# Performance work log

Hardware: AMD Instinct MI355X
Metric: run time of the kernel (lower is better)

## Reference

```python
import jax, jax.numpy as jnp
import numpy as np

AUDIO_DIM, TEXT_DIM, HIDDEN_DIM = 512, 768, 512
B, AUDIO_LEN, TEXT_LEN = 8, 2048, 512


def setup_inputs() -> dict:
    key = jax.random.key(0)
    ks = jax.random.split(key, 9)
    audio_features = jax.random.normal(ks[0], (B, AUDIO_LEN, AUDIO_DIM), dtype=jnp.float32)
    text_features = jax.random.normal(ks[1], (B, TEXT_LEN, TEXT_DIM), dtype=jnp.float32)
    text_mask = jax.random.randint(ks[2], (B, TEXT_LEN), 0, 2).astype(jnp.int32)
    # Linear params (PyTorch default init scale ~ U(-1/sqrt(fan_in), 1/sqrt(fan_in)))
    def lin(kw, kb, fan_in, fan_out):
        bound = 1.0 / np.sqrt(fan_in)
        W = jax.random.uniform(kw, (fan_in, fan_out), minval=-bound, maxval=bound, dtype=jnp.float32)
        b = jax.random.uniform(kb, (fan_out,), minval=-bound, maxval=bound, dtype=jnp.float32)
        return W, b
    Wq, bq = lin(ks[3], ks[4], AUDIO_DIM, HIDDEN_DIM)
    Wk, bk = lin(ks[5], ks[6], TEXT_DIM, HIDDEN_DIM)
    Wv, bv = lin(ks[7], ks[8], TEXT_DIM, HIDDEN_DIM)
    return {
        "audio_features": audio_features,
        "text_features": text_features,
        "Wq": Wq, "bq": bq, "Wk": Wk, "bk": bk, "Wv": Wv, "bv": bv,
        "text_mask": text_mask,
    }


def reference(audio_features, text_features, Wq, bq, Wk, bk, Wv, bv, text_mask):
    scale = HIDDEN_DIM ** -0.5
    q = jnp.einsum("bad,dh->bah", audio_features, Wq) + bq  # (B, A, H)
    k = jnp.einsum("btd,dh->bth", text_features, Wk) + bk   # (B, T, H)
    v = jnp.einsum("btd,dh->bth", text_features, Wv) + bv   # (B, T, H)
    scores = jnp.einsum("bah,bth->bat", q, k) * scale        # (B, A, T)
    mask = text_mask[:, None, :]  # (B, 1, T)
    scores = jnp.where(mask == 0, -jnp.inf, scores)
    attn = jax.nn.softmax(scores, axis=-1)
    # dropout is identity in eval mode
    enhanced_audio = jnp.einsum("bat,bth->bah", attn, v)     # (B, A, H)
    return enhanced_audio
```

## Files before the change

### kernel.cpp

```cpp
#include <hip/hip_runtime.h>
#include <cstdint>
#include <cstddef>

#define AUDIO_DIM 512
#define TEXT_DIM  768
#define HIDDEN    512
#define BATCH     8
#define ALEN      2048
#define TLEN      512

typedef _Float16 half8 __attribute__((ext_vector_type(8)));
typedef _Float16 half4_t __attribute__((ext_vector_type(4)));
typedef float floatx4 __attribute__((ext_vector_type(4)));

#define AS1 __attribute__((address_space(1)))
#define AS3 __attribute__((address_space(3)))

__device__ __forceinline__ void gload_lds16(const void* g, void* l) {
    __builtin_amdgcn_global_load_lds((const AS1 void*)g, (AS3 void*)l, 16, 0, 0);
}

__device__ __forceinline__ int swz(int r) { return (r >> 1) & 3; }

#define VMCNT(N) asm volatile("s_waitcnt vmcnt(" #N ")" ::: "memory")

__global__ __launch_bounds__(256) void prep(
    const float* __restrict__ text,
    const float* __restrict__ Wq, const float* __restrict__ Wk,
    const float* __restrict__ Wv,
    _Float16* __restrict__ text_h,
    _Float16* __restrict__ Wq_t, _Float16* __restrict__ Wk_t,
    _Float16* __restrict__ Wv_t)
{
    __shared__ _Float16 tt[32 * 33];
    const int bid = blockIdx.x, tid = threadIdx.x;
    if (bid < 3072) {
        int i = bid * 256 + tid;
        floatx4 v = __builtin_nontemporal_load(&((const floatx4*)text)[i]);
        half4_t h;
        h.x = (_Float16)v.x; h.y = (_Float16)v.y; h.z = (_Float16)v.z; h.w = (_Float16)v.w;
        ((half4_t*)text_h)[i] = h;
    } else {
        const float* src; _Float16* dst; int R, lb;
        if (bid < 3328)      { lb = bid - 3072; src = Wq; dst = Wq_t; R = 512; }
        else if (bid < 3712) { lb = bid - 3328; src = Wk; dst = Wk_t; R = 768; }
        else                 { lb = bid - 3712; src = Wv; dst = Wv_t; R = 768; }
        const int C = 512;
        const int c0 = (lb & 15) * 32, r0 = (lb >> 4) * 32;
        const int tx = tid & 31, ty = tid >> 5;
#pragma unroll
        for (int i = 0; i < 4; i++) {
            int r = ty + i * 8;
            tt[r * 33 + tx] =
                (_Float16)__builtin_nontemporal_load(&src[(size_t)(r0 + r) * C + c0 + tx]);
        }
        __syncthreads();
#pragma unroll
        for (int i = 0; i < 4; i++) {
            int r = ty + i * 8;
            dst[(size_t)(c0 + r) * R + r0 + tx] = tt[tx * 33 + r];
        }
    }
}

template <bool OUT16, bool ROWBIAS, bool CVT_A>
__device__ __forceinline__ void gemm_body(
    const void* __restrict__ Avp, const _Float16* __restrict__ Bt,
    const float* __restrict__ bias, void* __restrict__ Cp,
    int N, int K, int m0, int n0, _Float16* Asm, _Float16* Bsm)
{
    const int tid = threadIdx.x;
    const int l = tid & 63, w = tid >> 6;
    const int wm = w >> 1, wn = w & 1;
    const int srow = l >> 2, sj = l & 3;
    const int q = l >> 4, c16 = l & 15;

    floatx4 acc[4][4] = {};

    for (int k0 = 0; k0 < K; k0 += 32) {
        if (k0) __syncthreads();
#pragma unroll
        for (int i = 0; i < 2; i++) {
            int rb = (w * 2 + i) * 16;
            int r = rb + srow;
            int cc = sj ^ swz(r);
            if constexpr (CVT_A) {
                const float* Af = (const float*)Avp;
                const float* s = &Af[(size_t)(m0 + r) * K + k0 + cc * 8];
                floatx4 v0 = __builtin_nontemporal_load((const floatx4*)s);
                floatx4 v1 = __builtin_nontemporal_load((const floatx4*)(s + 4));
                half8 h;
                h[0] = (_Float16)v0.x; h[1] = (_Float16)v0.y;
                h[2] = (_Float16)v0.z; h[3] = (_Float16)v0.w;
                h[4] = (_Float16)v1.x; h[5] = (_Float16)v1.y;
                h[6] = (_Float16)v1.z; h[7] = (_Float16)v1.w;
                *(half8*)&Asm[r * 32 + sj * 8] = h;
            } else {
                const _Float16* Ah = (const _Float16*)Avp;
                gload_lds16(Ah + (size_t)(m0 + r) * K + k0 + cc * 8, Asm + rb * 32);
            }
            gload_lds16(Bt + (size_t)(n0 + r) * K + k0 + cc * 8, Bsm + rb * 32);
        }
        __syncthreads();

        half8 af[4], bf[4];
#pragma unroll
        for (int t = 0; t < 4; t++) {
            int rA = wm * 64 + t * 16 + c16;
            af[t] = *(const half8*)&Asm[rA * 32 + ((q ^ swz(rA)) << 3)];
            int rB = wn * 64 + t * 16 + c16;
            bf[t] = *(const half8*)&Bsm[rB * 32 + ((q ^ swz(rB)) << 3)];
        }
#pragma unroll
        for (int mi = 0; mi < 4; mi++)
#pragma unroll
            for (int ni = 0; ni < 4; ni++)
                acc[mi][ni] = __builtin_amdgcn_mfma_f32_16x16x32_f16(
                    af[mi], bf[ni], acc[mi][ni], 0, 0, 0);
    }

    if (OUT16) {
        float bcol[4];
        float brow[4][4];
        if (!ROWBIAS) {
#pragma unroll
            for (int ni = 0; ni < 4; ni++)
                bcol[ni] = bias[n0 + wn * 64 + ni * 16 + c16];
        } else {
#pragma unroll
            for (int mi = 0; mi < 4; mi++) {
                float4 b4 = *(const float4*)&bias[m0 + wm * 64 + mi * 16 + q * 4];
                brow[mi][0] = b4.x; brow[mi][1] = b4.y;
                brow[mi][2] = b4.z; brow[mi][3] = b4.w;
            }
        }
        _Float16* C = (_Float16*)Cp;
#pragma unroll
        for (int ni = 0; ni < 4; ni++) {
            int col = n0 + wn * 64 + ni * 16 + c16;
#pragma unroll
            for (int mi = 0; mi < 4; mi++) {
                int row = m0 + wm * 64 + mi * 16 + q * 4;
#pragma unroll
                for (int r = 0; r < 4; r++) {
                    float b = ROWBIAS ? brow[mi][r] : bcol[ni];
                    C[(size_t)(row + r) * N + col] = (_Float16)(acc[mi][ni][r] + b);
                }
            }
        }
    } else {
        float* C = (float*)Cp;
#pragma unroll
        for (int ni = 0; ni < 4; ni++) {
            int col = n0 + wn * 64 + ni * 16 + c16;
#pragma unroll
            for (int mi = 0; mi < 4; mi++) {
                int row = m0 + wm * 64 + mi * 16 + q * 4;
#pragma unroll
                for (int r = 0; r < 4; r++)
                    C[(size_t)(row + r) * N + col] = acc[mi][ni][r];
            }
        }
    }
}

__global__ __launch_bounds__(256, 3) void qkv_gemm(
    const float* __restrict__ audio, const _Float16* __restrict__ text_h,
    const _Float16* __restrict__ Wq_t, const _Float16* __restrict__ Wk_t,
    const _Float16* __restrict__ Wv_t,
    const float* __restrict__ bq, const float* __restrict__ bk,
    const float* __restrict__ bv,
    _Float16* __restrict__ Qh, _Float16* __restrict__ Kh,
    _Float16* __restrict__ Vt)
{
    __shared__ __align__(16) _Float16 Asm[128 * 32];
    __shared__ __align__(16) _Float16 Bsm[128 * 32];
    const int bid = blockIdx.x;
    if (bid < 512) {
        int t = (bid & 7) * 64 + (bid >> 3);
        gemm_body<true, false, true>(audio, Wq_t, bq, Qh, 512, 512,
                                     (t >> 2) * 128, (t & 3) * 128, Asm, Bsm);
    } else if (bid < 640) {
        int s = bid - 512;
        int t = (s & 7) * 16 + (s >> 3);
        gemm_body<true, false, false>(text_h, Wk_t, bk, Kh, 512, 768,
                                      (t >> 2) * 128, (t & 3) * 128, Asm, Bsm);
    } else {
        int s = bid - 640;
        int t = (s & 7) * 16 + (s >> 3);
        int z = t >> 4, by = (t >> 2) & 3, bx = t & 3;
        gemm_body<true, true, false>(Wv_t, text_h + (size_t)z * 393216, bv,
                                     Vt + (size_t)z * 262144, 512, 768,
                                     by * 128, bx * 128, Asm, Bsm);
    }
}

#define STAGE64(SRC, K0, BUF)                                               \
    do {                                                                    \
        _Pragma("unroll")                                                   \
        for (int i_ = 0; i_ < 4; i_++) {                                    \
            int lr_ = i_ * 16 + srow;                                       \
            int cc_ = sj ^ swz(lr_);                                        \
            gload_lds16((SRC) + (size_t)(w * 64 + lr_) * HIDDEN + (K0) + cc_ * 8, \
                        &(BUF)[i_ * 512]);                                  \
        }                                                                   \
    } while (0)

__global__ __launch_bounds__(512, 2) void attn(
    const _Float16* __restrict__ Qh, const _Float16* __restrict__ Kh,
    const _Float16* __restrict__ Vt, const int* __restrict__ mask,
    float* __restrict__ out)
{
    __shared__ __align__(16) _Float16 QPs[64 * 512];
    __shared__ __align__(16) _Float16 Ks[8][2][64 * 32];
    __shared__ float red[8][64];
    __shared__ float red2[8][64];
    const int tid = threadIdx.x, l = tid & 63, w = tid >> 6;
    const int lin = blockIdx.x;
    const int tb = (lin & 7) * 32 + (lin >> 3);
    const int b = tb >> 5, a0 = (tb & 31) * 64;
    const _Float16* Qb = Qh + (size_t)(b * ALEN + a0) * HIDDEN;
    const _Float16* Kb = Kh + (size_t)b * TLEN * HIDDEN;
    const _Float16* Vb = Vt + (size_t)b * TLEN * HIDDEN;
    const int srow = l >> 2, sj = l & 3;
    const int q = l >> 4, c16 = l & 15;

    int mv[4];
#pragma unroll
    for (int ni = 0; ni < 4; ni++)
        mv[ni] = mask[b * TLEN + w * 64 + ni * 16 + c16];

#pragma unroll
    for (int i = 0; i < 8; i++) {
        int r = w * 8 + i;
        gload_lds16(Qb + (size_t)r * 512 + ((l ^ (r & 7)) << 3), &QPs[r * 512]);
    }
    STAGE64(Kb, 0, Ks[w][0]);
    STAGE64(Kb, 32, Ks[w][1]);
    __syncthreads();

    floatx4 acc[4][4] = {};
#pragma unroll
    for (int ks = 0; ks < 16; ks++) {
        const int k0 = ks * 32;
        if (ks == 15) { VMCNT(0); } else { VMCNT(4); }
        half8 af[4], bf[4];
        const _Float16* kb = &Ks[w][ks & 1][0];
#pragma unroll
        for (int t = 0; t < 4; t++) {
            int rA = t * 16 + c16;
            af[t] = *(const half8*)&QPs[rA * 512 + ((((k0 >> 3) + q) ^ (rA & 7)) << 3)];
            bf[t] = *(const half8*)&kb[rA * 32 + ((q ^ swz(rA)) << 3)];
        }
#pragma unroll
        for (int mi = 0; mi < 4; mi++)
#pragma unroll
            for (int ni = 0; ni < 4; ni++)
                acc[mi][ni] = __builtin_amdgcn_mfma_f32_16x16x32_f16(
                    af[mi], bf[ni], acc[mi][ni], 0, 0, 0);
        if (ks < 14) STAGE64(Kb, k0 + 64, Ks[w][ks & 1]);
    }

    STAGE64(Vb, 0, Ks[w][0]);
    STAGE64(Vb, 32, Ks[w][1]);

    const float scale = 0.044194173824159216f;
#pragma unroll
    for (int mi = 0; mi < 4; mi++)
#pragma unroll
        for (int ni = 0; ni < 4; ni++)
#pragma unroll
            for (int r = 0; r < 4; r++)
                acc[mi][ni][r] = mv[ni] ? acc[mi][ni][r] * scale : -1e30f;

    float mx[4][4];
#pragma unroll
    for (int mi = 0; mi < 4; mi++)
#pragma unroll
        for (int r = 0; r < 4; r++) {
            float m = -1e30f;
#pragma unroll
            for (int ni = 0; ni < 4; ni++) m = fmaxf(m, acc[mi][ni][r]);
#pragma unroll
            for (int off = 1; off <= 8; off <<= 1) m = fmaxf(m, __shfl_xor(m, off));
            mx[mi][r] = m;
        }
    if (c16 == 0)
#pragma unroll
        for (int mi = 0; mi < 4; mi++)
#pragma unroll
            for (int r = 0; r < 4; r++) red[w][mi * 16 + q * 4 + r] = mx[mi][r];
    __syncthreads();
#pragma unroll
    for (int mi = 0; mi < 4; mi++)
#pragma unroll
        for (int r = 0; r < 4; r++) {
            int row = mi * 16 + q * 4 + r;
            float m = red[0][row];
#pragma unroll
            for (int ww = 1; ww < 8; ww++) m = fmaxf(m, red[ww][row]);
            mx[mi][r] = m;
        }

    float sm[4][4];
#pragma unroll
    for (int mi = 0; mi < 4; mi++)
#pragma unroll
        for (int r = 0; r < 4; r++) {
            float s = 0.f;
#pragma unroll
            for (int ni = 0; ni < 4; ni++) {
                float e = __expf(acc[mi][ni][r] - mx[mi][r]);
                acc[mi][ni][r] = e;
                s += e;
            }
#pragma unroll
            for (int off = 1; off <= 8; off <<= 1) s += __shfl_xor(s, off);
            sm[mi][r] = s;
        }
    if (c16 == 0)
#pragma unroll
        for (int mi = 0; mi < 4; mi++)
#pragma unroll
            for (int r = 0; r < 4; r++) red2[w][mi * 16 + q * 4 + r] = sm[mi][r];
    __syncthreads();

    _Float16* Ps = QPs;
#pragma unroll
    for (int mi = 0; mi < 4; mi++)
#pragma unroll
        for (int r = 0; r < 4; r++) {
            int row = mi * 16 + q * 4 + r;
            float s = red2[0][row];
#pragma unroll
            for (int ww = 1; ww < 8; ww++) s += red2[ww][row];
            float inv = 1.f / s;
#pragma unroll
            for (int ni = 0; ni < 4; ni++) {
                int col = w * 64 + ni * 16 + c16;
                Ps[row * 512 + ((((col >> 3) ^ (row & 7)) << 3) + (col & 7))] =
                    (_Float16)(acc[mi][ni][r] * inv);
            }
        }
    __syncthreads();

    floatx4 oacc[4][4] = {};
#pragma unroll
    for (int ts = 0; ts < 16; ts++) {
        const int t0 = ts * 32;
        if (ts == 15) { VMCNT(0); } else { VMCNT(4); }
        half8 af[4], bf[4];
        const _Float16* vb = &Ks[w][ts & 1][0];
#pragma unroll
        for (int t = 0; t < 4; t++) {
            int rA = t * 16 + c16;
            af[t] = *(const half8*)&Ps[rA * 512 + ((((t0 >> 3) + q) ^ (rA & 7)) << 3)];
            bf[t] = *(const half8*)&vb[rA * 32 + ((q ^ swz(rA)) << 3)];
        }
#pragma unroll
        for (int mi = 0; mi < 4; mi++)
#pragma unroll
            for (int ni = 0; ni < 4; ni++)
                oacc[mi][ni] = __builtin_amdgcn_mfma_f32_16x16x32_f16(
                    af[mi], bf[ni], oacc[mi][ni], 0, 0, 0);
        if (ts < 14) STAGE64(Vb, t0 + 64, Ks[w][ts & 1]);
    }

    float* Ob = out + (size_t)(b * ALEN + a0) * HIDDEN;
#pragma unroll
    for (int ni = 0; ni < 4; ni++) {
        int col = w * 64 + ni * 16 + c16;
#pragma unroll
        for (int mi = 0; mi < 4; mi++) {
            int row = mi * 16 + q * 4;
#pragma unroll
            for (int r = 0; r < 4; r++)
                __builtin_nontemporal_store(oacc[mi][ni][r],
                                            &Ob[(size_t)(row + r) * HIDDEN + col]);
        }
    }
}

extern "C" void kernel_launch(void* const* d_in, const int* in_sizes, int n_in,
                              void* d_out, int out_size, void* d_ws, size_t ws_size,
                              hipStream_t stream)
{
    const float* audio = (const float*)d_in[0];
    const float* text  = (const float*)d_in[1];
    const float* Wq    = (const float*)d_in[2];
    const float* bq    = (const float*)d_in[3];
    const float* Wk    = (const float*)d_in[4];
    const float* bk    = (const float*)d_in[5];
    const float* Wv    = (const float*)d_in[6];
    const float* bv    = (const float*)d_in[7];
    const int*   maskp = (const int*)d_in[8];
    float* out = (float*)d_out;

    _Float16* Qh = (_Float16*)d_out + (size_t)8388608;

    _Float16* ws16   = (_Float16*)d_ws;
    _Float16* text_h = ws16;
    _Float16* Wq_t   = text_h + 3145728;
    _Float16* Wk_t   = Wq_t + 262144;
    _Float16* Wv_t   = Wk_t + 393216;
    _Float16* Kh     = Wv_t + 393216;
    _Float16* Vt     = Kh + 2097152;

    prep<<<4096, 256, 0, stream>>>(text, Wq, Wk, Wv,
                                   text_h, Wq_t, Wk_t, Wv_t);
    qkv_gemm<<<768, 256, 0, stream>>>(audio, text_h, Wq_t, Wk_t, Wv_t,
                                      bq, bk, bv, Qh, Kh, Vt);
    attn<<<256, 512, 0, stream>>>(Qh, Kh, Vt, maskp, out);
}
```

Baseline: 167.5 us.

## Use 128x256 tiles for Q projection and pack K/V tiles two per block

```diff
diff --git a/kernel.cpp b/kernel.cpp
--- a/kernel.cpp
+++ b/kernel.cpp
@@ -63,13 +63,12 @@
     }
 }
 
-template <bool OUT16, bool ROWBIAS, bool CVT_A>
+template <bool OUT16, bool ROWBIAS>
 __device__ __forceinline__ void gemm_body(
-    const void* __restrict__ Avp, const _Float16* __restrict__ Bt,
+    const _Float16* __restrict__ A, const _Float16* __restrict__ Bt,
     const float* __restrict__ bias, void* __restrict__ Cp,
-    int N, int K, int m0, int n0, _Float16* Asm, _Float16* Bsm)
-{
-    const int tid = threadIdx.x;
+    int N, int K, int m0, int n0, _Float16* Asm, _Float16* Bsm, int tid)
+{
     const int l = tid & 63, w = tid >> 6;
     const int wm = w >> 1, wn = w & 1;
     const int srow = l >> 2, sj = l & 3;
@@ -84,21 +83,7 @@
             int rb = (w * 2 + i) * 16;
             int r = rb + srow;
             int cc = sj ^ swz(r);
-            if constexpr (CVT_A) {
-                const float* Af = (const float*)Avp;
-                const float* s = &Af[(size_t)(m0 + r) * K + k0 + cc * 8];
-                floatx4 v0 = __builtin_nontemporal_load((const floatx4*)s);
-                floatx4 v1 = __builtin_nontemporal_load((const floatx4*)(s + 4));
-                half8 h;
-                h[0] = (_Float16)v0.x; h[1] = (_Float16)v0.y;
-                h[2] = (_Float16)v0.z; h[3] = (_Float16)v0.w;
-                h[4] = (_Float16)v1.x; h[5] = (_Float16)v1.y;
-                h[6] = (_Float16)v1.z; h[7] = (_Float16)v1.w;
-                *(half8*)&Asm[r * 32 + sj * 8] = h;
-            } else {
-                const _Float16* Ah = (const _Float16*)Avp;
-                gload_lds16(Ah + (size_t)(m0 + r) * K + k0 + cc * 8, Asm + rb * 32);
-            }
+            gload_lds16(A + (size_t)(m0 + r) * K + k0 + cc * 8, Asm + rb * 32);
             gload_lds16(Bt + (size_t)(n0 + r) * K + k0 + cc * 8, Bsm + rb * 32);
         }
         __syncthreads();
@@ -164,7 +149,76 @@
     }
 }
 
-__global__ __launch_bounds__(256, 3) void qkv_gemm(
+__device__ __forceinline__ void q_gemm512(
+    const float* __restrict__ audio, const _Float16* __restrict__ Wq_t,
+    const float* __restrict__ bias, _Float16* __restrict__ Qh,
+    int m0, int n0, _Float16* As, _Float16* Bs, int tid)
+{
+    const int l = tid & 63, w = tid >> 6;
+    const int wm = w >> 2, wn = w & 3;
+    const int srow = l >> 2, sj = l & 3;
+    const int q = l >> 4, c16 = l & 15;
+    const int arow = tid >> 2, asj = tid & 3;
+    const int acc_ = asj ^ swz(arow);
+
+    floatx4 acc[4][4] = {};
+
+    for (int k0 = 0; k0 < 512; k0 += 32) {
+        if (k0) __syncthreads();
+        {
+            const float* s = &audio[(size_t)(m0 + arow) * 512 + k0 + acc_ * 8];
+            floatx4 v0 = __builtin_nontemporal_load((const floatx4*)s);
+            floatx4 v1 = __builtin_nontemporal_load((const floatx4*)(s + 4));
+            half8 h;
+            h[0] = (_Float16)v0.x; h[1] = (_Float16)v0.y;
+            h[2] = (_Float16)v0.z; h[3] = (_Float16)v0.w;
+            h[4] = (_Float16)v1.x; h[5] = (_Float16)v1.y;
+            h[6] = (_Float16)v1.z; h[7] = (_Float16)v1.w;
+            *(half8*)&As[arow * 32 + asj * 8] = h;
+        }
+#pragma unroll
+        for (int i = 0; i < 2; i++) {
+            int rb = (w * 2 + i) * 16;
+            int r = rb + srow;
+            int cc = sj ^ swz(r);
+            gload_lds16(Wq_t + (size_t)(n0 + r) * 512 + k0 + cc * 8, Bs + rb * 32);
+        }
+        __syncthreads();
+
+        half8 af[4], bf[4];
+#pragma unroll
+        for (int t = 0; t < 4; t++) {
+            int rA = wm * 64 + t * 16 + c16;
+            af[t] = *(const half8*)&As[rA * 32 + ((q ^ swz(rA)) << 3)];
+            int rB = wn * 64 + t * 16 + c16;
+            bf[t] = *(const half8*)&Bs[rB * 32 + ((q ^ swz(rB)) << 3)];
+        }
+#pragma unroll
+        for (int mi = 0; mi < 4; mi++)
+#pragma unroll
+            for (int ni = 0; ni < 4; ni++)
+                acc[mi][ni] = __builtin_amdgcn_mfma_f32_16x16x32_f16(
+                    af[mi], bf[ni], acc[mi][ni], 0, 0, 0);
+    }
+
+    float bcol[4];
+#pragma unroll
+    for (int ni = 0; ni < 4; ni++)
+        bcol[ni] = bias[n0 + wn * 64 + ni * 16 + c16];
+#pragma unroll
+    for (int ni = 0; ni < 4; ni++) {
+        int col = n0 + wn * 64 + ni * 16 + c16;
+#pragma unroll
+        for (int mi = 0; mi < 4; mi++) {
+            int row = m0 + wm * 64 + mi * 16 + q * 4;
+#pragma unroll
+            for (int r = 0; r < 4; r++)
+                Qh[(size_t)(row + r) * 512 + col] = (_Float16)(acc[mi][ni][r] + bcol[ni]);
+        }
+    }
+}
+
+__global__ __launch_bounds__(512, 2) void qkv_gemm(
     const float* __restrict__ audio, const _Float16* __restrict__ text_h,
     const _Float16* __restrict__ Wq_t, const _Float16* __restrict__ Wk_t,
     const _Float16* __restrict__ Wv_t,
@@ -173,25 +227,30 @@
     _Float16* __restrict__ Qh, _Float16* __restrict__ Kh,
     _Float16* __restrict__ Vt)
 {
-    __shared__ __align__(16) _Float16 Asm[128 * 32];
-    __shared__ __align__(16) _Float16 Bsm[128 * 32];
-    const int bid = blockIdx.x;
-    if (bid < 512) {
-        int t = (bid & 7) * 64 + (bid >> 3);
-        gemm_body<true, false, true>(audio, Wq_t, bq, Qh, 512, 512,
-                                     (t >> 2) * 128, (t & 3) * 128, Asm, Bsm);
-    } else if (bid < 640) {
-        int s = bid - 512;
-        int t = (s & 7) * 16 + (s >> 3);
-        gemm_body<true, false, false>(text_h, Wk_t, bk, Kh, 512, 768,
-                                      (t >> 2) * 128, (t & 3) * 128, Asm, Bsm);
+    __shared__ __align__(16) _Float16 smem[16384];
+    const int bid = blockIdx.x, tid = threadIdx.x;
+    if (bid < 256) {
+        int j = (bid & 7) * 32 + (bid >> 3);
+        q_gemm512(audio, Wq_t, bq, Qh, (j >> 1) * 128, (j & 1) * 256,
+                  smem, smem + 4096, tid);
+    } else if (bid < 320) {
+        int p = bid - 256;
+        int p2 = (p & 7) * 8 + (p >> 3);
+        int h = tid >> 8;
+        int t = 2 * p2 + h;
+        gemm_body<true, false>(text_h, Wk_t, bk, Kh, 512, 768,
+                               (t >> 2) * 128, (t & 3) * 128,
+                               smem + h * 8192, smem + h * 8192 + 4096, tid & 255);
     } else {
-        int s = bid - 640;
-        int t = (s & 7) * 16 + (s >> 3);
+        int p = bid - 320;
+        int p2 = (p & 7) * 8 + (p >> 3);
+        int h = tid >> 8;
+        int t = 2 * p2 + h;
         int z = t >> 4, by = (t >> 2) & 3, bx = t & 3;
-        gemm_body<true, true, false>(Wv_t, text_h + (size_t)z * 393216, bv,
-                                     Vt + (size_t)z * 262144, 512, 768,
-                                     by * 128, bx * 128, Asm, Bsm);
+        gemm_body<true, true>(Wv_t, text_h + (size_t)z * 393216, bv,
+                              Vt + (size_t)z * 262144, 512, 768,
+                              by * 128, bx * 128,
+                              smem + h * 8192, smem + h * 8192 + 4096, tid & 255);
     }
 }
 
@@ -408,7 +467,7 @@
 
     prep<<<4096, 256, 0, stream>>>(text, Wq, Wk, Wv,
                                    text_h, Wq_t, Wk_t, Wv_t);
-    qkv_gemm<<<768, 256, 0, stream>>>(audio, text_h, Wq_t, Wk_t, Wv_t,
+    qkv_gemm<<<384, 512, 0, stream>>>(audio, text_h, Wq_t, Wk_t, Wv_t,
                                       bq, bk, bv, Qh, Kh, Vt);
     attn<<<256, 512, 0, stream>>>(Qh, Kh, Vt, maskp, out);
 }
```

Measured after the change: 169.4 us. No clear change (+1.1%).
